# Optimization experiments

Hardware: AMD Instinct MI355X
Metric: run time of the kernel (lower is better)

The kernel has to match this reference:

```python
import jax, jax.numpy as jnp
import numpy as np

N = 50000
E = 500000
D = 64
H = 8
HD = D // H
CLAMP = 5.0


def _ln(x, g, b):
    m = x.mean(-1, keepdims=True)
    v = x.var(-1, keepdims=True)
    return (x - m) / jnp.sqrt(v + 1e-5) * g + b


def setup_inputs() -> dict:
    key = jax.random.key(0)
    ks = jax.random.split(key, 24)
    s = 0.1
    inp = {
        'x': jax.random.normal(ks[0], (N, D), jnp.float32),
        'edge_attr': jax.random.normal(ks[1], (E, D), jnp.float32),
        'log_deg': jnp.log1p(jax.random.uniform(ks[2], (N,), jnp.float32) * 64.0),
        'Wq': jax.random.normal(ks[3], (D, D), jnp.float32) * s,
        'bq': jnp.zeros((D,), jnp.float32),
        'Wk': jax.random.normal(ks[4], (D, D), jnp.float32) * s,
        'bk': jnp.zeros((D,), jnp.float32),
        'Wv': jax.random.normal(ks[5], (D, D), jnp.float32) * s,
        'bv': jnp.zeros((D,), jnp.float32),
        'We': jax.random.normal(ks[6], (D, 2 * D), jnp.float32) * s,
        'be': jnp.zeros((2 * D,), jnp.float32),
        'Aw': jax.random.normal(ks[7], (HD, H, 1), jnp.float32) * s,
        'VeRow': jax.random.normal(ks[8], (HD, H, HD), jnp.float32) * s,
        'deg_coef': jax.random.normal(ks[9], (1, D, 2), jnp.float32) * s,
        'Woh': jax.random.normal(ks[10], (D, D), jnp.float32) * s,
        'boh': jnp.zeros((D,), jnp.float32),
        'Woe': jax.random.normal(ks[11], (D, D), jnp.float32) * s,
        'boe': jnp.zeros((D,), jnp.float32),
        'ln1h_g': jnp.ones((D,), jnp.float32),
        'ln1h_b': jnp.zeros((D,), jnp.float32),
        'ln1e_g': jnp.ones((D,), jnp.float32),
        'ln1e_b': jnp.zeros((D,), jnp.float32),
        'W1': jax.random.normal(ks[12], (D, 2 * D), jnp.float32) * s,
        'b1': jnp.zeros((2 * D,), jnp.float32),
        'W2': jax.random.normal(ks[13], (2 * D, D), jnp.float32) * s,
        'b2': jnp.zeros((D,), jnp.float32),
        'ln2h_g': jnp.ones((D,), jnp.float32),
        'ln2h_b': jnp.zeros((D,), jnp.float32),
        'edge_index': jax.random.randint(ks[14], (2, E), 0, N, dtype=jnp.int32),
    }
    return inp


def reference(x, edge_attr, log_deg, Wq, bq, Wk, bk, Wv, bv, We, be, Aw, VeRow,
              deg_coef, Woh, boh, Woe, boe, ln1h_g, ln1h_b, ln1e_g, ln1e_b,
              W1, b1, W2, b2, ln2h_g, ln2h_b, edge_index):
    n = x.shape[0]
    src, dst = edge_index[0], edge_index[1]
    # node projections [N, H, HD]
    Qh = (x @ Wq + bq).reshape(n, H, HD)
    Kh = (x @ Wk + bk).reshape(n, H, HD)
    Vh = (x @ Wv + bv).reshape(n, H, HD)
    # edge projection -> per-edge multiplicative / additive terms
    Ee = (edge_attr @ We + be).reshape(-1, H, 2 * HD)
    Ew, Eb = Ee[..., :HD], Ee[..., HD:]
    # gather + score transform (signed-sqrt)
    s = (Kh[src] + Qh[dst]) * Ew
    s = jnp.sqrt(jax.nn.relu(s) + 1e-8) - jnp.sqrt(jax.nn.relu(-s) + 1e-8)
    s = s + Eb  # [E, H, HD], attn_act is Identity
    e_t = s
    wE = s.reshape(s.shape[0], H * HD)
    # contract to scalar attn logits per (edge, head)
    a = jnp.einsum('ehd,dhc->ehc', s, Aw)[..., 0]  # [E, H]
    a = jnp.clip(a, -CLAMP, CLAMP)
    # segment softmax over destination nodes
    amax = jax.ops.segment_max(a, dst, num_segments=n)
    amax = jnp.where(jnp.isfinite(amax), amax, 0.0)
    ex = jnp.exp(a - amax[dst])
    den = jax.ops.segment_sum(ex, dst, num_segments=n)
    attn = ex / (den[dst] + 1e-16)  # [E, H]
    # message + scatter-sum aggregation
    wV = jax.ops.segment_sum(Vh[src] * attn[..., None], dst, num_segments=n)
    # edge enhancement
    rowV = jax.ops.segment_sum(e_t * attn[..., None], dst, num_segments=n)
    wV = wV + jnp.einsum('nhd,dhc->nhc', rowV, VeRow)
    h = wV.reshape(n, H * HD)
    # degree scaler
    h = h * deg_coef[:, :, 0] + (h * log_deg[:, None]) * deg_coef[:, :, 1]
    h = h @ Woh + boh
    e = wE @ Woe + boe
    # residual + layernorm
    h = _ln(x + h, ln1h_g, ln1h_b)
    e = _ln(edge_attr + e, ln1e_g, ln1e_b)
    # FFN block
    h2 = jax.nn.relu(h @ W1 + b1) @ W2 + b2
    h = _ln(h + h2, ln2h_g, ln2h_b)
    return h, e
```

## Files before the change

### kernel.cpp

```cpp
#include <hip/hip_runtime.h>
#include <hip/hip_bf16.h>

#define NN 50000
#define NE 500000
#define NTILES ((NE + 63) / 64)
#define NTILEN ((NN + 63) / 64)
#define SCAN_BLK 49

typedef __hip_bfloat16 bf16;
typedef short s16x8 __attribute__((ext_vector_type(8)));
typedef float f32x4 __attribute__((ext_vector_type(4)));

__device__ __forceinline__ float wave_sum(float v) {
#pragma unroll
  for (int o = 32; o >= 1; o >>= 1) v += __shfl_xor(v, o);
  return v;
}

__device__ __forceinline__ unsigned short f2bf(float f) {
  __hip_bfloat16 h = __float2bfloat16(f);
  return __builtin_bit_cast(unsigned short, h);
}

__device__ __forceinline__ float bf2f(unsigned short u) {
  union { unsigned u; float f; } v; v.u = ((unsigned)u) << 16;
  return v.f;
}

__global__ __launch_bounds__(256, 4) void qkv_kernel(
    const float* __restrict__ x,
    const float* __restrict__ Wq, const float* __restrict__ bq,
    const float* __restrict__ Wk, const float* __restrict__ bk,
    const float* __restrict__ Wv, const float* __restrict__ bv,
    unsigned short* __restrict__ Qh, unsigned short* __restrict__ Kh,
    unsigned short* __restrict__ Vh) {
  __shared__ unsigned short sXhi[64][72];
  __shared__ unsigned short sXlo[64][72];
  const int tid = threadIdx.x;
  const int lane = tid & 63;
  const int w = tid >> 6;
  const int c15 = lane & 15;
  const int q = lane >> 4;
  const int klo = q * 8;
  const int g16 = lane >> 4;
  const int l16 = lane & 15;

  const float* Wsel[3] = {Wq, Wk, Wv};
  const float* bsel[3] = {bq, bk, bv};
  unsigned short* osel[3] = {Qh, Kh, Vh};
  const int col = w * 16 + c15;

  s16x8 bf[3][2];
#pragma unroll
  for (int j = 0; j < 3; ++j) {
#pragma unroll
    for (int kh = 0; kh < 2; ++kh) {
      s16x8 tmp;
#pragma unroll
      for (int i = 0; i < 8; ++i) tmp[i] = (short)f2bf(Wsel[j][(kh * 32 + klo + i) * 64 + col]);
      bf[j][kh] = tmp;
    }
  }
  float bias_r[3];
#pragma unroll
  for (int j = 0; j < 3; ++j) bias_r[j] = bsel[j][col];

  for (int T = blockIdx.x; T < NTILEN; T += gridDim.x) {
    const int N0 = T * 64;
#pragma unroll
    for (int it = 0; it < 4; ++it) {
      int r = it * 16 + w * 4 + g16;
      int n = N0 + r;
      float4 xv = {0.f, 0.f, 0.f, 0.f};
      if (n < NN) xv = *(const float4*)&x[(size_t)n * 64 + l16 * 4];
      ushort4 h4, l4;
      h4.x = f2bf(xv.x); l4.x = f2bf(xv.x - bf2f(h4.x));
      h4.y = f2bf(xv.y); l4.y = f2bf(xv.y - bf2f(h4.y));
      h4.z = f2bf(xv.z); l4.z = f2bf(xv.z - bf2f(h4.z));
      h4.w = f2bf(xv.w); l4.w = f2bf(xv.w - bf2f(h4.w));
      *(ushort4*)&sXhi[r][l16 * 4] = h4;
      *(ushort4*)&sXlo[r][l16 * 4] = l4;
    }
    __syncthreads();

    f32x4 acc[4][3];
#pragma unroll
    for (int m = 0; m < 4; ++m)
#pragma unroll
      for (int j = 0; j < 3; ++j) acc[m][j] = (f32x4){0.f, 0.f, 0.f, 0.f};
#pragma unroll
    for (int m = 0; m < 4; ++m) {
      s16x8 h0 = *(const s16x8*)&sXhi[16 * m + c15][klo];
      s16x8 h1 = *(const s16x8*)&sXhi[16 * m + c15][klo + 32];
      s16x8 l0 = *(const s16x8*)&sXlo[16 * m + c15][klo];
      s16x8 l1 = *(const s16x8*)&sXlo[16 * m + c15][klo + 32];
#pragma unroll
      for (int j = 0; j < 3; ++j) {
        acc[m][j] = __builtin_amdgcn_mfma_f32_16x16x32_bf16(h0, bf[j][0], acc[m][j], 0, 0, 0);
        acc[m][j] = __builtin_amdgcn_mfma_f32_16x16x32_bf16(h1, bf[j][1], acc[m][j], 0, 0, 0);
        acc[m][j] = __builtin_amdgcn_mfma_f32_16x16x32_bf16(l0, bf[j][0], acc[m][j], 0, 0, 0);
        acc[m][j] = __builtin_amdgcn_mfma_f32_16x16x32_bf16(l1, bf[j][1], acc[m][j], 0, 0, 0);
      }
    }
#pragma unroll
    for (int m = 0; m < 4; ++m) {
#pragma unroll
      for (int j = 0; j < 3; ++j) {
#pragma unroll
        for (int i = 0; i < 4; ++i) {
          int n = N0 + 16 * m + q * 4 + i;
          if (n < NN) osel[j][(size_t)n * 64 + col] = f2bf(acc[m][j][i] + bias_r[j]);
        }
      }
    }
    __syncthreads();
  }
}

__global__ __launch_bounds__(256) void hist_kernel(const int* __restrict__ eidx, int* __restrict__ cnt) {
  int i = blockIdx.x * 256 + threadIdx.x;
  if (i < NE) atomicAdd(&cnt[eidx[NE + i]], 1);
}

__global__ __launch_bounds__(256) void scan1_kernel(const int* __restrict__ cnt, int* __restrict__ bsum) {
  __shared__ int wsum[4];
  const int t = threadIdx.x;
  const int base = blockIdx.x * 1024 + t * 4;
  int s = 0;
#pragma unroll
  for (int j = 0; j < 4; j++) {
    int i = base + j;
    if (i < NN) s += cnt[i];
  }
#pragma unroll
  for (int o = 1; o < 64; o <<= 1) s += __shfl_xor(s, o);
  if ((t & 63) == 0) wsum[t >> 6] = s;
  __syncthreads();
  if (t == 0) bsum[blockIdx.x] = wsum[0] + wsum[1] + wsum[2] + wsum[3];
}

__global__ __launch_bounds__(64) void scan2_kernel(int* __restrict__ bsum, int* __restrict__ rs) {
  const int t = threadIdx.x;
  int v = (t < SCAN_BLK) ? bsum[t] : 0;
  int s = v;
#pragma unroll
  for (int o = 1; o < 64; o <<= 1) {
    int u = __shfl_up(s, o);
    if (t >= o) s += u;
  }
  if (t < SCAN_BLK) bsum[t] = s - v;
  if (t == 63) rs[NN] = s;
}

__global__ __launch_bounds__(256) void scan3_kernel(int* __restrict__ cnt, const int* __restrict__ bsum,
                                                    int* __restrict__ rs) {
  __shared__ int wsum[4];
  const int t = threadIdx.x;
  const int lane = t & 63, w = t >> 6;
  const int base = blockIdx.x * 1024 + t * 4;
  int v[4];
  int s = 0;
#pragma unroll
  for (int j = 0; j < 4; j++) {
    int i = base + j;
    v[j] = (i < NN) ? cnt[i] : 0;
    s += v[j];
  }
  int inc = s;
#pragma unroll
  for (int o = 1; o < 64; o <<= 1) {
    int u = __shfl_up(inc, o);
    if (lane >= o) inc += u;
  }
  int ex = inc - s;
  int wtot = __shfl(inc, 63);
  if (lane == 0) wsum[w] = wtot;
  __syncthreads();
  int woff = 0;
  for (int i = 0; i < w; i++) woff += wsum[i];
  int off = bsum[blockIdx.x] + woff + ex;
#pragma unroll
  for (int j = 0; j < 4; j++) {
    int i = base + j;
    if (i < NN) {
      rs[i] = off;
      cnt[i] = off;
      off += v[j];
    }
  }
}

__global__ __launch_bounds__(256) void scatter_kernel(const int* __restrict__ eidx,
                                                      int* __restrict__ cur,
                                                      int* __restrict__ slot,
                                                      int* __restrict__ srcs) {
  int e = blockIdx.x * 256 + threadIdx.x;
  if (e < NE) {
    int src = eidx[e];
    int dst = eidx[NE + e];
    int p = atomicAdd(&cur[dst], 1);
    slot[e] = p;
    srcs[p] = src;
  }
}

__global__ __launch_bounds__(256, 5) void edge_kernel(
    const float* __restrict__ ea,
    const float* __restrict__ We, const float* __restrict__ be,
    const float* __restrict__ Aw,
    const float* __restrict__ Woe, const float* __restrict__ boe,
    const float* __restrict__ ge, const float* __restrict__ bbe,
    const unsigned short* __restrict__ Qh, const unsigned short* __restrict__ Kh,
    const int* __restrict__ eidx, const int* __restrict__ slot,
    bf16* __restrict__ sE, float* __restrict__ exE, float* __restrict__ out_e) {
  __shared__ unsigned short sA[64][72];
  __shared__ unsigned short sKQ[64][72];
  __shared__ int sSlot[64];

  const int tid = threadIdx.x;
  const int lane = tid & 63;
  const int w = tid >> 6;
  const int c15 = lane & 15;
  const int q = lane >> 4;
  const int klo = q * 8;
  const int g16 = lane >> 4;
  const int l16 = lane & 15;

  s16x8 b1f[2][2], b2f[4][2];
#pragma unroll
  for (int nt = 0; nt < 2; ++nt) {
    int col = (2 * w + nt) * 16 + c15;
#pragma unroll
    for (int kh = 0; kh < 2; ++kh) {
      s16x8 tmp;
#pragma unroll
      for (int i = 0; i < 8; ++i) tmp[i] = (short)f2bf(We[(kh * 32 + klo + i) * 128 + col]);
      b1f[nt][kh] = tmp;
    }
  }
#pragma unroll
  for (int n = 0; n < 4; ++n) {
    int col = n * 16 + c15;
#pragma unroll
    for (int kh = 0; kh < 2; ++kh) {
      s16x8 tmp;
#pragma unroll
      for (int i = 0; i < 8; ++i) tmp[i] = (short)f2bf(Woe[(kh * 32 + klo + i) * 64 + col]);
      b2f[n][kh] = tmp;
    }
  }
  float be_r[2], aw_r[2];
#pragma unroll
  for (int nt = 0; nt < 2; ++nt) {
    be_r[nt] = be[(2 * w + nt) * 16 + c15];
    aw_r[nt] = Aw[(c15 & 7) * 8 + (2 * w + nt)];
  }
  float boe_r[4], ge_r[4], bbe_r[4];
#pragma unroll
  for (int n = 0; n < 4; ++n) {
    boe_r[n] = boe[n * 16 + c15];
    ge_r[n] = ge[n * 16 + c15];
    bbe_r[n] = bbe[n * 16 + c15];
  }

  for (int T = blockIdx.x; T < NTILES; T += gridDim.x) {
    const int E0 = T * 64;
#pragma unroll
    for (int it = 0; it < 4; ++it) {
      int r = it * 16 + w * 4 + g16;
      int e = E0 + r;
      float4 av = {0.f, 0.f, 0.f, 0.f};
      ushort4 kv = {0, 0, 0, 0};
      ushort4 qv = {0, 0, 0, 0};
      int sl = 0;
      if (e < NE) {
        av = *(const float4*)&ea[(size_t)e * 64 + l16 * 4];
        int sn = eidx[e], dn = eidx[NE + e];
        kv = *(const ushort4*)&Kh[(size_t)sn * 64 + l16 * 4];
        qv = *(const ushort4*)&Qh[(size_t)dn * 64 + l16 * 4];
        sl = slot[e];
      }
      ushort4 a4, k4;
      a4.x = f2bf(av.x); a4.y = f2bf(av.y); a4.z = f2bf(av.z); a4.w = f2bf(av.w);
      k4.x = f2bf(bf2f(kv.x) + bf2f(qv.x));
      k4.y = f2bf(bf2f(kv.y) + bf2f(qv.y));
      k4.z = f2bf(bf2f(kv.z) + bf2f(qv.z));
      k4.w = f2bf(bf2f(kv.w) + bf2f(qv.w));
      *(ushort4*)&sA[r][l16 * 4] = a4;
      *(ushort4*)&sKQ[r][l16 * 4] = k4;
      if (l16 == 0) sSlot[r] = sl;
    }
    __syncthreads();

    f32x4 acc[4][2];
#pragma unroll
    for (int m = 0; m < 4; ++m)
#pragma unroll
      for (int nt = 0; nt < 2; ++nt) acc[m][nt] = (f32x4){0.f, 0.f, 0.f, 0.f};
#pragma unroll
    for (int m = 0; m < 4; ++m) {
      s16x8 a0 = *(const s16x8*)&sA[16 * m + c15][klo];
      s16x8 a1 = *(const s16x8*)&sA[16 * m + c15][klo + 32];
#pragma unroll
      for (int nt = 0; nt < 2; ++nt) {
        acc[m][nt] = __builtin_amdgcn_mfma_f32_16x16x32_bf16(a0, b1f[nt][0], acc[m][nt], 0, 0, 0);
        acc[m][nt] = __builtin_amdgcn_mfma_f32_16x16x32_bf16(a1, b1f[nt][1], acc[m][nt], 0, 0, 0);
      }
    }
#pragma unroll
    for (int m = 0; m < 4; ++m) {
#pragma unroll
      for (int nt = 0; nt < 2; ++nt) {
        const int t = 2 * w + nt;
#pragma unroll
        for (int i = 0; i < 4; ++i) {
          int row = 16 * m + q * 4 + i;
          float s = acc[m][nt][i] + be_r[nt];
          float kq = bf2f(sKQ[row][t * 8 + (c15 & 7)]);
          float ks = kq * s;
          float g;
          if (c15 < 8)
            g = copysignf(sqrtf(fabsf(ks) + 1e-8f) - 1e-4f, ks);
          else
            g = s;
          float et = g + __shfl_xor(g, 8);
          if (c15 < 8) sKQ[row][t * 8 + c15] = f2bf(et);
          float p = et * aw_r[nt];
          p += __shfl_xor(p, 1);
          p += __shfl_xor(p, 2);
          p += __shfl_xor(p, 4);
          if (c15 == 0 && (E0 + row) < NE) {
            p = fminf(fmaxf(p, -5.f), 5.f);
            exE[(size_t)sSlot[row] * 8 + t] = expf(p);
          }
        }
      }
    }
    __syncthreads();

    const int rbase = 16 * w;
    f32x4 acc2[4];
#pragma unroll
    for (int n = 0; n < 4; ++n) acc2[n] = (f32x4){0.f, 0.f, 0.f, 0.f};
    {
      s16x8 wa0 = *(const s16x8*)&sKQ[rbase + c15][klo];
      s16x8 wa1 = *(const s16x8*)&sKQ[rbase + c15][klo + 32];
#pragma unroll
      for (int n = 0; n < 4; ++n) {
        acc2[n] = __builtin_amdgcn_mfma_f32_16x16x32_bf16(wa0, b2f[n][0], acc2[n], 0, 0, 0);
        acc2[n] = __builtin_amdgcn_mfma_f32_16x16x32_bf16(wa1, b2f[n][1], acc2[n], 0, 0, 0);
      }
    }
#pragma unroll
    for (int i = 0; i < 4; ++i) {
      int row = rbase + q * 4 + i;
      int e = E0 + row;
      bool val = e < NE;
      float r1[4];
      float sum = 0.f;
#pragma unroll
      for (int n = 0; n < 4; ++n) {
        float eav = bf2f(sA[row][n * 16 + c15]);
        r1[n] = eav + acc2[n][i] + boe_r[n];
        sum += r1[n];
      }
      sum += __shfl_xor(sum, 1);
      sum += __shfl_xor(sum, 2);
      sum += __shfl_xor(sum, 4);
      sum += __shfl_xor(sum, 8);
      float mean = sum * 0.015625f;
      float dv[4];
      float vs = 0.f;
#pragma unroll
      for (int n = 0; n < 4; ++n) {
        dv[n] = r1[n] - mean;
        vs += dv[n] * dv[n];
      }
      vs += __shfl_xor(vs, 1);
      vs += __shfl_xor(vs, 2);
      vs += __shfl_xor(vs, 4);
      vs += __shfl_xor(vs, 8);
      float inv = rsqrtf(vs * 0.015625f + 1e-5f);
#pragma unroll
      for (int n = 0; n < 4; ++n)
        if (val) out_e[(size_t)e * 64 + n * 16 + c15] = dv[n] * inv * ge_r[n] + bbe_r[n];
    }
#pragma unroll 4
    for (int rr = 0; rr < 16; ++rr) {
      int row = rbase + rr;
      int e = E0 + row;
      if (e < NE && lane < 32) {
        unsigned v2 = *(const unsigned*)&sKQ[row][lane * 2];
        *(unsigned*)((unsigned short*)sE + (size_t)sSlot[row] * 64 + lane * 2) = v2;
      }
    }
    __syncthreads();
  }
}

__global__ __launch_bounds__(256) void node_gather_kernel(
    const unsigned short* __restrict__ Vh, const bf16* __restrict__ sE,
    const float* __restrict__ exE,
    const int* __restrict__ srcs, const int* __restrict__ rs,
    const float* __restrict__ VeRow, const float* __restrict__ deg_coef,
    const float* __restrict__ log_deg, float* __restrict__ hA) {
  __shared__ float VeL[512];
  __shared__ float dcL[128];
  const int tid = threadIdx.x;
  for (int i = tid; i < 512; i += 256) VeL[i] = VeRow[i];
  if (tid < 128) dcL[tid] = deg_coef[tid];
  __syncthreads();
  const int lane = tid & 63;
  const int n = blockIdx.x * 4 + (tid >> 6);
  if (n >= NN) return;
  const int beg = rs[n], end = rs[n + 1];
  const int h = lane >> 3;
  float den = 0.f, wv = 0.f, rv = 0.f;
#pragma unroll 2
  for (int i = beg; i < end; i++) {
    float ex = exE[(size_t)i * 8 + h];
    float v = bf2f(Vh[(size_t)srcs[i] * 64 + lane]);
    float sv = __bfloat162float(sE[(size_t)i * 64 + lane]);
    den += ex;
    wv = fmaf(ex, v, wv);
    rv = fmaf(ex, sv, rv);
  }
  float inv = 1.f / (den + 1e-16f);
  wv *= inv;
  rv *= inv;
#pragma unroll
  for (int d2 = 0; d2 < 8; d2++) {
    float r = __shfl(rv, (lane & 56) + d2);
    wv = fmaf(r, VeL[d2 * 64 + lane], wv);
  }
  float ld = log_deg[n];
  hA[(size_t)n * 64 + lane] = wv * (dcL[2 * lane] + ld * dcL[2 * lane + 1]);
}

__global__ __launch_bounds__(256) void node_epi1_kernel(
    const float* __restrict__ x,
    const float* __restrict__ Woh, const float* __restrict__ boh,
    const float* __restrict__ g1, const float* __restrict__ bb1,
    float* __restrict__ hio) {
  __shared__ float WohL[4096];
  __shared__ float sb[192];
  const int tid = threadIdx.x;
  for (int i = tid; i < 4096; i += 256) WohL[i] = Woh[i];
  if (tid < 64) { sb[tid] = boh[tid]; sb[64 + tid] = g1[tid]; sb[128 + tid] = bb1[tid]; }
  __syncthreads();
  const int lane = tid & 63;
  const int n0 = (blockIdx.x * 4 + (tid >> 6)) * 4;
  float hv[4], acc[4];
#pragma unroll
  for (int j = 0; j < 4; j++) {
    hv[j] = (n0 + j < NN) ? hio[(size_t)(n0 + j) * 64 + lane] : 0.f;
    acc[j] = sb[lane];
  }
#pragma unroll 8
  for (int k = 0; k < 64; k++) {
    float w = WohL[k * 64 + lane];
#pragma unroll
    for (int j = 0; j < 4; j++) acc[j] = fmaf(__shfl(hv[j], k), w, acc[j]);
  }
#pragma unroll
  for (int j = 0; j < 4; j++) {
    if (n0 + j >= NN) continue;
    float r1 = x[(size_t)(n0 + j) * 64 + lane] + acc[j];
    float m = wave_sum(r1) * 0.015625f;
    float dv = r1 - m;
    float var = wave_sum(dv * dv) * 0.015625f;
    hio[(size_t)(n0 + j) * 64 + lane] = dv * rsqrtf(var + 1e-5f) * sb[64 + lane] + sb[128 + lane];
  }
}

__global__ __launch_bounds__(256, 4) void node_epi2_kernel(
    const float* __restrict__ W1, const float* __restrict__ b1,
    const float* __restrict__ W2, const float* __restrict__ b2,
    const float* __restrict__ g2, const float* __restrict__ bb2,
    float* __restrict__ hio) {
  extern __shared__ float sm[];
  float* W1L = sm;
  float* W2L = sm + 8192;
  float* sb = sm + 16384;
  const int tid = threadIdx.x;
  for (int i = tid; i < 8192; i += 256) { W1L[i] = W1[i]; W2L[i] = W2[i]; }
  if (tid < 128) sb[tid] = b1[tid];
  if (tid < 64) { sb[128 + tid] = b2[tid]; sb[192 + tid] = g2[tid]; sb[256 + tid] = bb2[tid]; }
  __syncthreads();
  const int lane = tid & 63;
  const int n0 = (blockIdx.x * 4 + (tid >> 6)) * 4;
  float h1[4];
#pragma unroll
  for (int j = 0; j < 4; j++)
    h1[j] = (n0 + j < NN) ? hio[(size_t)(n0 + j) * 64 + lane] : 0.f;
  float ua[4], ub[4];
#pragma unroll
  for (int j = 0; j < 4; j++) { ua[j] = sb[lane]; ub[j] = sb[64 + lane]; }
#pragma unroll 4
  for (int k = 0; k < 64; k++) {
    float wa = W1L[k * 128 + lane];
    float wb = W1L[k * 128 + 64 + lane];
#pragma unroll
    for (int j = 0; j < 4; j++) {
      float w = __shfl(h1[j], k);
      ua[j] = fmaf(w, wa, ua[j]);
      ub[j] = fmaf(w, wb, ub[j]);
    }
  }
  float a2[4];
#pragma unroll
  for (int j = 0; j < 4; j++) {
    ua[j] = fmaxf(ua[j], 0.f);
    ub[j] = fmaxf(ub[j], 0.f);
    a2[j] = sb[128 + lane];
  }
#pragma unroll 4
  for (int k = 0; k < 64; k++) {
    float wa = W2L[k * 64 + lane];
    float wb = W2L[(64 + k) * 64 + lane];
#pragma unroll
    for (int j = 0; j < 4; j++) {
      a2[j] = fmaf(__shfl(ua[j], k), wa, a2[j]);
      a2[j] = fmaf(__shfl(ub[j], k), wb, a2[j]);
    }
  }
#pragma unroll
  for (int j = 0; j < 4; j++) {
    if (n0 + j >= NN) continue;
    float r2 = h1[j] + a2[j];
    float m = wave_sum(r2) * 0.015625f;
    float dv = r2 - m;
    float var = wave_sum(dv * dv) * 0.015625f;
    hio[(size_t)(n0 + j) * 64 + lane] = dv * rsqrtf(var + 1e-5f) * sb[192 + lane] + sb[256 + lane];
  }
}

extern "C" void kernel_launch(void* const* d_in, const int* in_sizes, int n_in,
                              void* d_out, int out_size, void* d_ws, size_t ws_size,
                              hipStream_t stream) {
  const float* x = (const float*)d_in[0];
  const float* ea = (const float*)d_in[1];
  const float* log_deg = (const float*)d_in[2];
  const float* Wq = (const float*)d_in[3];
  const float* bq = (const float*)d_in[4];
  const float* Wk = (const float*)d_in[5];
  const float* bk = (const float*)d_in[6];
  const float* Wv = (const float*)d_in[7];
  const float* bv = (const float*)d_in[8];
  const float* We = (const float*)d_in[9];
  const float* be = (const float*)d_in[10];
  const float* Aw = (const float*)d_in[11];
  const float* VeRow = (const float*)d_in[12];
  const float* deg_coef = (const float*)d_in[13];
  const float* Woh = (const float*)d_in[14];
  const float* boh = (const float*)d_in[15];
  const float* Woe = (const float*)d_in[16];
  const float* boe = (const float*)d_in[17];
  const float* g1h = (const float*)d_in[18];
  const float* b1h = (const float*)d_in[19];
  const float* g1e = (const float*)d_in[20];
  const float* b1e = (const float*)d_in[21];
  const float* W1 = (const float*)d_in[22];
  const float* b1 = (const float*)d_in[23];
  const float* W2 = (const float*)d_in[24];
  const float* b2 = (const float*)d_in[25];
  const float* g2h = (const float*)d_in[26];
  const float* b2h = (const float*)d_in[27];
  const int* eidx = (const int*)d_in[28];

  char* p = (char*)d_ws;
  unsigned short* Qh = (unsigned short*)p; p += (size_t)NN * 64 * 2;
  unsigned short* Kh = (unsigned short*)p; p += (size_t)NN * 64 * 2;
  unsigned short* Vh = (unsigned short*)p; p += (size_t)NN * 64 * 2;
  bf16* sE = (bf16*)p;  p += (size_t)NE * 64 * 2;
  float* exE = (float*)p; p += (size_t)NE * 8 * 4;
  int* cnt = (int*)p;   p += ((size_t)NN * 4 + 255) & ~(size_t)255;
  int* rs = (int*)p;    p += (((size_t)NN + 1) * 4 + 255) & ~(size_t)255;
  int* slot = (int*)p;  p += (size_t)NE * 4;
  int* srcs = (int*)p;  p += (size_t)NE * 4;
  int* bsum = (int*)p;  p += ((size_t)SCAN_BLK * 4 + 255) & ~(size_t)255;
  if ((size_t)(p - (char*)d_ws) > ws_size) return;

  float* out_h = (float*)d_out;
  float* out_e = out_h + (size_t)NN * 64;

  hipMemsetAsync(cnt, 0, NN * sizeof(int), stream);
  qkv_kernel<<<782, 256, 0, stream>>>(x, Wq, bq, Wk, bk, Wv, bv, Qh, Kh, Vh);
  hist_kernel<<<(NE + 255) / 256, 256, 0, stream>>>(eidx, cnt);
  scan1_kernel<<<SCAN_BLK, 256, 0, stream>>>(cnt, bsum);
  scan2_kernel<<<1, 64, 0, stream>>>(bsum, rs);
  scan3_kernel<<<SCAN_BLK, 256, 0, stream>>>(cnt, bsum, rs);
  scatter_kernel<<<(NE + 255) / 256, 256, 0, stream>>>(eidx, cnt, slot, srcs);
  edge_kernel<<<1280, 256, 0, stream>>>(ea, We, be, Aw, Woe, boe, g1e, b1e,
                                        Qh, Kh, eidx, slot, sE, exE, out_e);
  node_gather_kernel<<<(NN + 3) / 4, 256, 0, stream>>>(Vh, sE, exE, srcs, rs, VeRow,
                                                       deg_coef, log_deg, out_h);
  node_epi1_kernel<<<(NN + 15) / 16, 256, 0, stream>>>(x, Woh, boh, g1h, b1h, out_h);
  node_epi2_kernel<<<(NN + 15) / 16, 256, 16704 * 4, stream>>>(W1, b1, W2, b2, g2h, b2h, out_h);
}
```

Baseline: 514.7 us.

## Process edges in CSR order in edge kernel and fuse Woh epilogue into gather

The edge kernel now walks edges in destination-sorted (CSR) order using eid/srcs/dsts arrays, so the sE and exE writes become contiguous and Qh reads mostly repeat the same destination. The random-access cost moves to the edge_attr reads and the out_e writes, which are now indexed by the original edge id. Separately, the node_epi1 Woh projection, residual and layernorm are fused into node_gather_kernel, removing one kernel launch and a round trip of h through global memory. The gather kernel in exchange loads the 16 KB Woh matrix into LDS for every 4-node block, which may reduce occupancy and adds load work.

```diff
diff --git a/kernel.cpp b/kernel.cpp
--- a/kernel.cpp
+++ b/kernel.cpp
@@ -192,15 +192,17 @@
 
 __global__ __launch_bounds__(256) void scatter_kernel(const int* __restrict__ eidx,
                                                       int* __restrict__ cur,
-                                                      int* __restrict__ slot,
-                                                      int* __restrict__ srcs) {
+                                                      int* __restrict__ eid,
+                                                      int* __restrict__ srcs,
+                                                      int* __restrict__ dsts) {
   int e = blockIdx.x * 256 + threadIdx.x;
   if (e < NE) {
     int src = eidx[e];
     int dst = eidx[NE + e];
     int p = atomicAdd(&cur[dst], 1);
-    slot[e] = p;
+    eid[p] = e;
     srcs[p] = src;
+    dsts[p] = dst;
   }
 }
 
@@ -211,11 +213,11 @@
     const float* __restrict__ Woe, const float* __restrict__ boe,
     const float* __restrict__ ge, const float* __restrict__ bbe,
     const unsigned short* __restrict__ Qh, const unsigned short* __restrict__ Kh,
-    const int* __restrict__ eidx, const int* __restrict__ slot,
+    const int* __restrict__ eid, const int* __restrict__ srcs, const int* __restrict__ dsts,
     bf16* __restrict__ sE, float* __restrict__ exE, float* __restrict__ out_e) {
   __shared__ unsigned short sA[64][72];
   __shared__ unsigned short sKQ[64][72];
-  __shared__ int sSlot[64];
+  __shared__ int sEid[64];
 
   const int tid = threadIdx.x;
   const int lane = tid & 63;
@@ -268,17 +270,16 @@
 #pragma unroll
     for (int it = 0; it < 4; ++it) {
       int r = it * 16 + w * 4 + g16;
-      int e = E0 + r;
+      int pos = E0 + r;
       float4 av = {0.f, 0.f, 0.f, 0.f};
       ushort4 kv = {0, 0, 0, 0};
       ushort4 qv = {0, 0, 0, 0};
-      int sl = 0;
-      if (e < NE) {
-        av = *(const float4*)&ea[(size_t)e * 64 + l16 * 4];
-        int sn = eidx[e], dn = eidx[NE + e];
-        kv = *(const ushort4*)&Kh[(size_t)sn * 64 + l16 * 4];
-        qv = *(const ushort4*)&Qh[(size_t)dn * 64 + l16 * 4];
-        sl = slot[e];
+      int ed = 0;
+      if (pos < NE) {
+        ed = eid[pos];
+        av = *(const float4*)&ea[(size_t)ed * 64 + l16 * 4];
+        kv = *(const ushort4*)&Kh[(size_t)srcs[pos] * 64 + l16 * 4];
+        qv = *(const ushort4*)&Qh[(size_t)dsts[pos] * 64 + l16 * 4];
       }
       ushort4 a4, k4;
       a4.x = f2bf(av.x); a4.y = f2bf(av.y); a4.z = f2bf(av.z); a4.w = f2bf(av.w);
@@ -288,7 +289,7 @@
       k4.w = f2bf(bf2f(kv.w) + bf2f(qv.w));
       *(ushort4*)&sA[r][l16 * 4] = a4;
       *(ushort4*)&sKQ[r][l16 * 4] = k4;
-      if (l16 == 0) sSlot[r] = sl;
+      if (l16 == 0) sEid[r] = ed;
     }
     __syncthreads();
 
@@ -331,7 +332,7 @@
           p += __shfl_xor(p, 4);
           if (c15 == 0 && (E0 + row) < NE) {
             p = fminf(fmaxf(p, -5.f), 5.f);
-            exE[(size_t)sSlot[row] * 8 + t] = expf(p);
+            exE[(size_t)(E0 + row) * 8 + t] = expf(p);
           }
         }
       }
@@ -354,8 +355,9 @@
 #pragma unroll
     for (int i = 0; i < 4; ++i) {
       int row = rbase + q * 4 + i;
-      int e = E0 + row;
-      bool val = e < NE;
+      int pos = E0 + row;
+      bool val = pos < NE;
+      int ed = sEid[row];
       float r1[4];
       float sum = 0.f;
 #pragma unroll
@@ -383,15 +385,15 @@
       float inv = rsqrtf(vs * 0.015625f + 1e-5f);
 #pragma unroll
       for (int n = 0; n < 4; ++n)
-        if (val) out_e[(size_t)e * 64 + n * 16 + c15] = dv[n] * inv * ge_r[n] + bbe_r[n];
+        if (val) out_e[(size_t)ed * 64 + n * 16 + c15] = dv[n] * inv * ge_r[n] + bbe_r[n];
     }
 #pragma unroll 4
     for (int rr = 0; rr < 16; ++rr) {
       int row = rbase + rr;
-      int e = E0 + row;
-      if (e < NE && lane < 32) {
+      int pos = E0 + row;
+      if (pos < NE && lane < 32) {
         unsigned v2 = *(const unsigned*)&sKQ[row][lane * 2];
-        *(unsigned*)((unsigned short*)sE + (size_t)sSlot[row] * 64 + lane * 2) = v2;
+        *(unsigned*)((unsigned short*)sE + (size_t)pos * 64 + lane * 2) = v2;
       }
     }
     __syncthreads();
@@ -403,12 +405,20 @@
     const float* __restrict__ exE,
     const int* __restrict__ srcs, const int* __restrict__ rs,
     const float* __restrict__ VeRow, const float* __restrict__ deg_coef,
-    const float* __restrict__ log_deg, float* __restrict__ hA) {
+    const float* __restrict__ log_deg,
+    const float* __restrict__ x,
+    const float* __restrict__ Woh, const float* __restrict__ boh,
+    const float* __restrict__ g1, const float* __restrict__ bb1,
+    float* __restrict__ h1out) {
   __shared__ float VeL[512];
   __shared__ float dcL[128];
+  __shared__ float WohL[4096];
+  __shared__ float sb[192];
   const int tid = threadIdx.x;
   for (int i = tid; i < 512; i += 256) VeL[i] = VeRow[i];
   if (tid < 128) dcL[tid] = deg_coef[tid];
+  for (int i = tid; i < 4096; i += 256) WohL[i] = Woh[i];
+  if (tid < 64) { sb[tid] = boh[tid]; sb[64 + tid] = g1[tid]; sb[128 + tid] = bb1[tid]; }
   __syncthreads();
   const int lane = tid & 63;
   const int n = blockIdx.x * 4 + (tid >> 6);
@@ -434,43 +444,15 @@
     wv = fmaf(r, VeL[d2 * 64 + lane], wv);
   }
   float ld = log_deg[n];
-  hA[(size_t)n * 64 + lane] = wv * (dcL[2 * lane] + ld * dcL[2 * lane + 1]);
-}
-
-__global__ __launch_bounds__(256) void node_epi1_kernel(
-    const float* __restrict__ x,
-    const float* __restrict__ Woh, const float* __restrict__ boh,
-    const float* __restrict__ g1, const float* __restrict__ bb1,
-    float* __restrict__ hio) {
-  __shared__ float WohL[4096];
-  __shared__ float sb[192];
-  const int tid = threadIdx.x;
-  for (int i = tid; i < 4096; i += 256) WohL[i] = Woh[i];
-  if (tid < 64) { sb[tid] = boh[tid]; sb[64 + tid] = g1[tid]; sb[128 + tid] = bb1[tid]; }
-  __syncthreads();
-  const int lane = tid & 63;
-  const int n0 = (blockIdx.x * 4 + (tid >> 6)) * 4;
-  float hv[4], acc[4];
-#pragma unroll
-  for (int j = 0; j < 4; j++) {
-    hv[j] = (n0 + j < NN) ? hio[(size_t)(n0 + j) * 64 + lane] : 0.f;
-    acc[j] = sb[lane];
-  }
+  float hv = wv * (dcL[2 * lane] + ld * dcL[2 * lane + 1]);
+  float acc = sb[lane];
 #pragma unroll 8
-  for (int k = 0; k < 64; k++) {
-    float w = WohL[k * 64 + lane];
-#pragma unroll
-    for (int j = 0; j < 4; j++) acc[j] = fmaf(__shfl(hv[j], k), w, acc[j]);
-  }
-#pragma unroll
-  for (int j = 0; j < 4; j++) {
-    if (n0 + j >= NN) continue;
-    float r1 = x[(size_t)(n0 + j) * 64 + lane] + acc[j];
-    float m = wave_sum(r1) * 0.015625f;
-    float dv = r1 - m;
-    float var = wave_sum(dv * dv) * 0.015625f;
-    hio[(size_t)(n0 + j) * 64 + lane] = dv * rsqrtf(var + 1e-5f) * sb[64 + lane] + sb[128 + lane];
-  }
+  for (int k = 0; k < 64; k++) acc = fmaf(__shfl(hv, k), WohL[k * 64 + lane], acc);
+  float r1 = x[(size_t)n * 64 + lane] + acc;
+  float m = wave_sum(r1) * 0.015625f;
+  float dv = r1 - m;
+  float var = wave_sum(dv * dv) * 0.015625f;
+  h1out[(size_t)n * 64 + lane] = dv * rsqrtf(var + 1e-5f) * sb[64 + lane] + sb[128 + lane];
 }
 
 __global__ __launch_bounds__(256, 4) void node_epi2_kernel(
@@ -576,8 +558,9 @@
   float* exE = (float*)p; p += (size_t)NE * 8 * 4;
   int* cnt = (int*)p;   p += ((size_t)NN * 4 + 255) & ~(size_t)255;
   int* rs = (int*)p;    p += (((size_t)NN + 1) * 4 + 255) & ~(size_t)255;
-  int* slot = (int*)p;  p += (size_t)NE * 4;
+  int* eid = (int*)p;   p += (size_t)NE * 4;
   int* srcs = (int*)p;  p += (size_t)NE * 4;
+  int* dsts = (int*)p;  p += (size_t)NE * 4;
   int* bsum = (int*)p;  p += ((size_t)SCAN_BLK * 4 + 255) & ~(size_t)255;
   if ((size_t)(p - (char*)d_ws) > ws_size) return;
 
@@ -590,11 +573,11 @@
   scan1_kernel<<<SCAN_BLK, 256, 0, stream>>>(cnt, bsum);
   scan2_kernel<<<1, 64, 0, stream>>>(bsum, rs);
   scan3_kernel<<<SCAN_BLK, 256, 0, stream>>>(cnt, bsum, rs);
-  scatter_kernel<<<(NE + 255) / 256, 256, 0, stream>>>(eidx, cnt, slot, srcs);
+  scatter_kernel<<<(NE + 255) / 256, 256, 0, stream>>>(eidx, cnt, eid, srcs, dsts);
   edge_kernel<<<1280, 256, 0, stream>>>(ea, We, be, Aw, Woe, boe, g1e, b1e,
-                                        Qh, Kh, eidx, slot, sE, exE, out_e);
+                                        Qh, Kh, eid, srcs, dsts, sE, exE, out_e);
   node_gather_kernel<<<(NN + 3) / 4, 256, 0, stream>>>(Vh, sE, exE, srcs, rs, VeRow,
-                                                       deg_coef, log_deg, out_h);
-  node_epi1_kernel<<<(NN + 15) / 16, 256, 0, stream>>>(x, Woh, boh, g1h, b1h, out_h);
+                                                       deg_coef, log_deg,
+                                                       x, Woh, boh, g1h, b1h, out_h);
   node_epi2_kernel<<<(NN + 15) / 16, 256, 16704 * 4, stream>>>(W1, b1, W2, b2, g2h, b2h, out_h);
 }
```

Result: slower. 530.0 us (+3.0%).

## Prefetch next edge tile into registers and fuse Woh/LayerNorm into node gather

Applied to the files above, without the earlier changes.

The edge kernel now issues the global loads for the next tile (edge_attr, gathered K/Q rows, slot) into registers right after the shared-memory barrier, so they overlap with the current tile's MFMA work. The node gather kernel also absorbs the Woh projection, residual and first LayerNorm, which removes a separate launch and the intermediate write and re-read of the node features. The cost is higher register pressure in the edge kernel. The gather kernel gains a per-block 16KB Woh shared-memory load for only 4 nodes per block, which may reduce occupancy.

```diff
diff --git a/kernel.cpp b/kernel.cpp
--- a/kernel.cpp
+++ b/kernel.cpp
@@ -263,34 +263,52 @@
     bbe_r[n] = bbe[n * 16 + c15];
   }
 
-  for (int T = blockIdx.x; T < NTILES; T += gridDim.x) {
+  float4 avR[4];
+  ushort4 kvR[4], qvR[4];
+  int slR[4];
+
+  auto LOAD = [&](int T) {
     const int E0 = T * 64;
 #pragma unroll
     for (int it = 0; it < 4; ++it) {
       int r = it * 16 + w * 4 + g16;
       int e = E0 + r;
-      float4 av = {0.f, 0.f, 0.f, 0.f};
-      ushort4 kv = {0, 0, 0, 0};
-      ushort4 qv = {0, 0, 0, 0};
-      int sl = 0;
+      avR[it] = (float4){0.f, 0.f, 0.f, 0.f};
+      kvR[it] = (ushort4){0, 0, 0, 0};
+      qvR[it] = (ushort4){0, 0, 0, 0};
+      slR[it] = 0;
       if (e < NE) {
-        av = *(const float4*)&ea[(size_t)e * 64 + l16 * 4];
+        avR[it] = *(const float4*)&ea[(size_t)e * 64 + l16 * 4];
         int sn = eidx[e], dn = eidx[NE + e];
-        kv = *(const ushort4*)&Kh[(size_t)sn * 64 + l16 * 4];
-        qv = *(const ushort4*)&Qh[(size_t)dn * 64 + l16 * 4];
-        sl = slot[e];
-      }
+        kvR[it] = *(const ushort4*)&Kh[(size_t)sn * 64 + l16 * 4];
+        qvR[it] = *(const ushort4*)&Qh[(size_t)dn * 64 + l16 * 4];
+        slR[it] = slot[e];
+      }
+    }
+  };
+
+  int T = blockIdx.x;
+  if (T < NTILES) LOAD(T);
+  for (; T < NTILES; T += gridDim.x) {
+    const int E0 = T * 64;
+#pragma unroll
+    for (int it = 0; it < 4; ++it) {
+      int r = it * 16 + w * 4 + g16;
       ushort4 a4, k4;
-      a4.x = f2bf(av.x); a4.y = f2bf(av.y); a4.z = f2bf(av.z); a4.w = f2bf(av.w);
-      k4.x = f2bf(bf2f(kv.x) + bf2f(qv.x));
-      k4.y = f2bf(bf2f(kv.y) + bf2f(qv.y));
-      k4.z = f2bf(bf2f(kv.z) + bf2f(qv.z));
-      k4.w = f2bf(bf2f(kv.w) + bf2f(qv.w));
+      a4.x = f2bf(avR[it].x); a4.y = f2bf(avR[it].y);
+      a4.z = f2bf(avR[it].z); a4.w = f2bf(avR[it].w);
+      k4.x = f2bf(bf2f(kvR[it].x) + bf2f(qvR[it].x));
+      k4.y = f2bf(bf2f(kvR[it].y) + bf2f(qvR[it].y));
+      k4.z = f2bf(bf2f(kvR[it].z) + bf2f(qvR[it].z));
+      k4.w = f2bf(bf2f(kvR[it].w) + bf2f(qvR[it].w));
       *(ushort4*)&sA[r][l16 * 4] = a4;
       *(ushort4*)&sKQ[r][l16 * 4] = k4;
-      if (l16 == 0) sSlot[r] = sl;
+      if (l16 == 0) sSlot[r] = slR[it];
     }
     __syncthreads();
+
+    int Tn = T + gridDim.x;
+    if (Tn < NTILES) LOAD(Tn);
 
     f32x4 acc[4][2];
 #pragma unroll
@@ -403,12 +421,20 @@
     const float* __restrict__ exE,
     const int* __restrict__ srcs, const int* __restrict__ rs,
     const float* __restrict__ VeRow, const float* __restrict__ deg_coef,
-    const float* __restrict__ log_deg, float* __restrict__ hA) {
+    const float* __restrict__ log_deg,
+    const float* __restrict__ x,
+    const float* __restrict__ Woh, const float* __restrict__ boh,
+    const float* __restrict__ g1, const float* __restrict__ bb1,
+    float* __restrict__ h1out) {
   __shared__ float VeL[512];
   __shared__ float dcL[128];
+  __shared__ float WohL[4096];
+  __shared__ float sb[192];
   const int tid = threadIdx.x;
   for (int i = tid; i < 512; i += 256) VeL[i] = VeRow[i];
   if (tid < 128) dcL[tid] = deg_coef[tid];
+  for (int i = tid; i < 4096; i += 256) WohL[i] = Woh[i];
+  if (tid < 64) { sb[tid] = boh[tid]; sb[64 + tid] = g1[tid]; sb[128 + tid] = bb1[tid]; }
   __syncthreads();
   const int lane = tid & 63;
   const int n = blockIdx.x * 4 + (tid >> 6);
@@ -434,43 +460,15 @@
     wv = fmaf(r, VeL[d2 * 64 + lane], wv);
   }
   float ld = log_deg[n];
-  hA[(size_t)n * 64 + lane] = wv * (dcL[2 * lane] + ld * dcL[2 * lane + 1]);
-}
-
-__global__ __launch_bounds__(256) void node_epi1_kernel(
-    const float* __restrict__ x,
-    const float* __restrict__ Woh, const float* __restrict__ boh,
-    const float* __restrict__ g1, const float* __restrict__ bb1,
-    float* __restrict__ hio) {
-  __shared__ float WohL[4096];
-  __shared__ float sb[192];
-  const int tid = threadIdx.x;
-  for (int i = tid; i < 4096; i += 256) WohL[i] = Woh[i];
-  if (tid < 64) { sb[tid] = boh[tid]; sb[64 + tid] = g1[tid]; sb[128 + tid] = bb1[tid]; }
-  __syncthreads();
-  const int lane = tid & 63;
-  const int n0 = (blockIdx.x * 4 + (tid >> 6)) * 4;
-  float hv[4], acc[4];
-#pragma unroll
-  for (int j = 0; j < 4; j++) {
-    hv[j] = (n0 + j < NN) ? hio[(size_t)(n0 + j) * 64 + lane] : 0.f;
-    acc[j] = sb[lane];
-  }
+  float hv = wv * (dcL[2 * lane] + ld * dcL[2 * lane + 1]);
+  float acc = sb[lane];
 #pragma unroll 8
-  for (int k = 0; k < 64; k++) {
-    float w = WohL[k * 64 + lane];
-#pragma unroll
-    for (int j = 0; j < 4; j++) acc[j] = fmaf(__shfl(hv[j], k), w, acc[j]);
-  }
-#pragma unroll
-  for (int j = 0; j < 4; j++) {
-    if (n0 + j >= NN) continue;
-    float r1 = x[(size_t)(n0 + j) * 64 + lane] + acc[j];
-    float m = wave_sum(r1) * 0.015625f;
-    float dv = r1 - m;
-    float var = wave_sum(dv * dv) * 0.015625f;
-    hio[(size_t)(n0 + j) * 64 + lane] = dv * rsqrtf(var + 1e-5f) * sb[64 + lane] + sb[128 + lane];
-  }
+  for (int k = 0; k < 64; k++) acc = fmaf(__shfl(hv, k), WohL[k * 64 + lane], acc);
+  float r1 = x[(size_t)n * 64 + lane] + acc;
+  float m = wave_sum(r1) * 0.015625f;
+  float dv = r1 - m;
+  float var = wave_sum(dv * dv) * 0.015625f;
+  h1out[(size_t)n * 64 + lane] = dv * rsqrtf(var + 1e-5f) * sb[64 + lane] + sb[128 + lane];
 }
 
 __global__ __launch_bounds__(256, 4) void node_epi2_kernel(
@@ -594,7 +592,7 @@
   edge_kernel<<<1280, 256, 0, stream>>>(ea, We, be, Aw, Woe, boe, g1e, b1e,
                                         Qh, Kh, eidx, slot, sE, exE, out_e);
   node_gather_kernel<<<(NN + 3) / 4, 256, 0, stream>>>(Vh, sE, exE, srcs, rs, VeRow,
-                                                       deg_coef, log_deg, out_h);
-  node_epi1_kernel<<<(NN + 15) / 16, 256, 0, stream>>>(x, Woh, boh, g1h, b1h, out_h);
+                                                       deg_coef, log_deg,
+                                                       x, Woh, boh, g1h, b1h, out_h);
   node_epi2_kernel<<<(NN + 15) / 16, 256, 16704 * 4, stream>>>(W1, b1, W2, b2, g2h, b2h, out_h);
 }
```

Result: slower. 703.9 us (+36.8%).
